# Kernel optimization log

Measured on AMD Instinct MI355X. Metric: run time of the kernel, lower is better.

The kernel has to match this reference:

```python
import jax, jax.numpy as jnp
import numpy as np

B, S, D, H = 16, 577, 1408, 16
HD = D // H  # 88


def setup_inputs() -> dict:
    key = jax.random.key(0)
    k1, k2, k3, k4, k5, k6 = jax.random.split(key, 6)
    hidden_states = jax.random.normal(k1, (B, S, D), dtype=jnp.float32)
    # realistic rotary table: cos/sin pairs stacked in last dim
    theta = jax.random.normal(k2, (S, HD // 2), dtype=jnp.float32)
    freqs_ci = jnp.stack([jnp.cos(theta), jnp.sin(theta)], axis=-1)  # (S, HD/2, 2)
    wqkv = jax.random.normal(k3, (3 * D, D), dtype=jnp.float32) * 0.02
    bqkv = jax.random.normal(k4, (3 * D,), dtype=jnp.float32) * 0.02
    wo = jax.random.normal(k5, (D, D), dtype=jnp.float32) * 0.02
    bo = jax.random.normal(k6, (D,), dtype=jnp.float32) * 0.02
    return {"hidden_states": hidden_states, "freqs_ci": freqs_ci,
            "wqkv": wqkv, "bqkv": bqkv, "wo": wo, "bo": bo}


def reference(hidden_states, freqs_ci, wqkv, bqkv, wo, bo):
    b, s, d = hidden_states.shape
    # fused QKV projection (torch Linear: x @ W.T + b)
    qkv = hidden_states @ wqkv.T + bqkv  # (B, S, 3D)
    q, k, v = jnp.split(qkv, 3, axis=-1)
    q = q.reshape(b, s, H, HD)
    k = k.reshape(b, s, H, HD)
    v = v.reshape(b, s, H, HD)

    cos = freqs_ci[..., 0][None, :, None, :]  # (1, S, 1, HD/2)
    sin = freqs_ci[..., 1][None, :, None, :]

    def rot(x):
        xr = x.reshape(b, s, H, HD // 2, 2)
        xe, xo = xr[..., 0], xr[..., 1]
        re = xe * cos - xo * sin
        ro = xe * sin + xo * cos
        return jnp.stack([re, ro], axis=-1).reshape(b, s, H, HD)

    q = rot(q)
    k = rot(k)

    scale = 1.0 / jnp.sqrt(jnp.float32(HD))  # SDPA default scaling
    scores = jnp.einsum('bqhd,bkhd->bhqk', q, k) * scale
    attn = jax.nn.softmax(scores, axis=-1)
    ctx = jnp.einsum('bhqk,bkhd->bqhd', attn, v).reshape(b, s, d)
    return ctx @ wo.T + bo
```

## Files before the change

kernel.cpp:

```cpp
#include <hip/hip_runtime.h>

typedef __attribute__((ext_vector_type(8))) __bf16 bf16x8;
typedef __attribute__((ext_vector_type(4))) float f32x4;
typedef __attribute__((ext_vector_type(4))) unsigned int uint4v;

#define B_ 16
#define S_ 577
#define D_ 1408
#define H_ 16
#define HD_ 88
#define MROWS (B_*S_)
#define N1 (3*D_)
#define K_ D_
#define KSTEPS 44
#define VT_LD 592
#define QSCALE 0.15379180809f

static __device__ __forceinline__ void async16(void* lds, const void* g) {
  __builtin_amdgcn_global_load_lds((const __attribute__((address_space(1))) void*)g,
                                   (__attribute__((address_space(3))) void*)lds, 16, 0, 0);
}

static __device__ __forceinline__ int xcd_swizzle(int orig, int nwg) {
  int xcd = orig & 7, lid = orig >> 3;
  int q = nwg >> 3, r = nwg & 7;
  return (xcd < r ? xcd * (q + 1) : r * (q + 1) + (xcd - r) * q) + lid;
}

__global__ void cast3_bf16_kernel(const float* __restrict__ s0, __bf16* __restrict__ d0, int n0,
                                  const float* __restrict__ s1, __bf16* __restrict__ d1, int n1,
                                  const float* __restrict__ s2, __bf16* __restrict__ d2, int n2) {
  int i = blockIdx.x * blockDim.x + threadIdx.x;
  const float* s; __bf16* d; int k;
  if (i < n0) { s = s0; d = d0; k = i; }
  else if (i < n0 + n1) { s = s1; d = d1; k = i - n0; }
  else if (i < n0 + n1 + n2) { s = s2; d = d2; k = i - n0 - n1; }
  else return;
  const float4 v = ((const float4*)s)[k];
  __bf16* p = d + (size_t)k * 4;
  p[0] = (__bf16)v.x; p[1] = (__bf16)v.y; p[2] = (__bf16)v.z; p[3] = (__bf16)v.w;
}

__launch_bounds__(256, 2)
__global__ void gemm_qkv_rope(const __bf16* __restrict__ A, const __bf16* __restrict__ Bm,
                              const float* __restrict__ bias, const float* __restrict__ freqs,
                              __bf16* __restrict__ Qb, __bf16* __restrict__ Kb,
                              __bf16* __restrict__ Vb) {
  __shared__ __bf16 As[2][128 * 32];
  __shared__ __bf16 Bs[2][128 * 32];
  const int tid = threadIdx.x;
  const int w = tid >> 6, l = tid & 63;
  const int wgid = xcd_swizzle(blockIdx.x, 33 * 73);
  int mt, nt;
  if (wgid < 2376) { int bnd = wgid / 132, r = wgid % 132; nt = r >> 2; mt = bnd * 4 + (r & 3); }
  else             { nt = wgid - 2376; mt = 72; }
  const int m0 = mt * 128, n0 = nt * 128;
  const int wr = w & 1, wc = w >> 1;
  const int M = MROWS, K = K_;

  f32x4 acc[4][4];
#pragma unroll
  for (int m = 0; m < 4; ++m)
#pragma unroll
    for (int n = 0; n < 4; ++n) acc[m][n] = (f32x4){0.f, 0.f, 0.f, 0.f};

  int arow0 = m0 + w * 32 + (l >> 2);      if (arow0 >= M) arow0 = M - 1;
  int arow1 = m0 + w * 32 + 16 + (l >> 2); if (arow1 >= M) arow1 = M - 1;
  const __bf16* ag0 = A + (size_t)arow0 * K + (l & 3) * 8;
  const __bf16* ag1 = A + (size_t)arow1 * K + (l & 3) * 8;
  const __bf16* bg0 = Bm + (size_t)(n0 + w * 32 + (l >> 2)) * K + (l & 3) * 8;
  const __bf16* bg1 = Bm + (size_t)(n0 + w * 32 + 16 + (l >> 2)) * K + (l & 3) * 8;

  auto stage = [&](int buf, int k0) {
    async16(&As[buf][(w * 32) * 32],      ag0 + k0);
    async16(&As[buf][(w * 32 + 16) * 32], ag1 + k0);
    async16(&Bs[buf][(w * 32) * 32],      bg0 + k0);
    async16(&Bs[buf][(w * 32 + 16) * 32], bg1 + k0);
  };

  stage(0, 0);
  __syncthreads();
  for (int t = 0; t < KSTEPS; ++t) {
    const int cur = t & 1;
    if (t < KSTEPS - 1) stage(cur ^ 1, (t + 1) * 32);
    bf16x8 a[4], b[4];
#pragma unroll
    for (int m = 0; m < 4; ++m)
      a[m] = *(const bf16x8*)&As[cur][(wr * 64 + m * 16 + (l & 15)) * 32 + (l >> 4) * 8];
#pragma unroll
    for (int n = 0; n < 4; ++n)
      b[n] = *(const bf16x8*)&Bs[cur][(wc * 64 + n * 16 + (l & 15)) * 32 + (l >> 4) * 8];
#pragma unroll
    for (int m = 0; m < 4; ++m)
#pragma unroll
      for (int n = 0; n < 4; ++n)
        acc[m][n] = __builtin_amdgcn_mfma_f32_16x16x32_bf16(a[m], b[n], acc[m][n], 0, 0, 0);
    __syncthreads();
  }

  const int sect = n0 / 1408;
  __bf16* dst = (sect == 0) ? Qb : (sect == 1 ? Kb : Vb);
  const float qs = (sect == 0) ? QSCALE : 1.f;
  int hN[4], dN[4], i2N[4];
  float bvN[4], sgnN[4];
#pragma unroll
  for (int n = 0; n < 4; ++n) {
    const int col = n0 + wc * 64 + n * 16 + (l & 15);
    const int cin = col - sect * 1408;
    hN[n] = cin / 88; dN[n] = cin - hN[n] * 88;
    bvN[n] = bias[col];
    i2N[n] = dN[n] & ~1;
    sgnN[n] = (dN[n] & 1) ? 1.f : -1.f;
  }
#pragma unroll
  for (int m = 0; m < 4; ++m) {
    const int rbase = m0 + wr * 64 + m * 16 + (l >> 4) * 4;
#pragma unroll
    for (int j = 0; j < 4; ++j) {
      const int r = rbase + j;
      const int s = r % 577;
      const int b = r / 577;
      const bool ok = r < MROWS;
      const float* frow = freqs + s * 88;
      __bf16* drow = dst + ((size_t)b * 16 * 577 + s) * 88;
#pragma unroll
      for (int n = 0; n < 4; ++n) {
        float val = acc[m][n][j] + bvN[n];
        float outv = val;
        if (sect < 2) {
          const float2 cs = *(const float2*)&frow[i2N[n]];
          const float p = __shfl_xor(val, 1);
          outv = (val * cs.x + sgnN[n] * p * cs.y) * qs;
        }
        if (ok) drow[(size_t)hN[n] * 50776 + dN[n]] = (__bf16)outv;
      }
    }
  }
}

__launch_bounds__(256, 2)
__global__ void gemm_out_bias(const __bf16* __restrict__ A, const __bf16* __restrict__ Bm,
                              const float* __restrict__ bias, float* __restrict__ C) {
  __shared__ __bf16 As[2][128 * 32];
  __shared__ __bf16 Bs[2][128 * 32];
  const int tid = threadIdx.x;
  const int w = tid >> 6, l = tid & 63;
  const int wgid = xcd_swizzle(blockIdx.x, 11 * 73);
  int mt, nt;
  if (wgid < 792) { int bnd = wgid / 44, r = wgid % 44; nt = r >> 2; mt = bnd * 4 + (r & 3); }
  else            { nt = wgid - 792; mt = 72; }
  const int m0 = mt * 128, n0 = nt * 128;
  const int wr = w & 1, wc = w >> 1;
  const int M = MROWS, N = D_, K = K_;

  f32x4 acc[4][4];
#pragma unroll
  for (int m = 0; m < 4; ++m)
#pragma unroll
    for (int n = 0; n < 4; ++n) acc[m][n] = (f32x4){0.f, 0.f, 0.f, 0.f};

  int arow0 = m0 + w * 32 + (l >> 2);      if (arow0 >= M) arow0 = M - 1;
  int arow1 = m0 + w * 32 + 16 + (l >> 2); if (arow1 >= M) arow1 = M - 1;
  const __bf16* ag0 = A + (size_t)arow0 * K + (l & 3) * 8;
  const __bf16* ag1 = A + (size_t)arow1 * K + (l & 3) * 8;
  const __bf16* bg0 = Bm + (size_t)(n0 + w * 32 + (l >> 2)) * K + (l & 3) * 8;
  const __bf16* bg1 = Bm + (size_t)(n0 + w * 32 + 16 + (l >> 2)) * K + (l & 3) * 8;

  auto stage = [&](int buf, int k0) {
    async16(&As[buf][(w * 32) * 32],      ag0 + k0);
    async16(&As[buf][(w * 32 + 16) * 32], ag1 + k0);
    async16(&Bs[buf][(w * 32) * 32],      bg0 + k0);
    async16(&Bs[buf][(w * 32 + 16) * 32], bg1 + k0);
  };

  stage(0, 0);
  __syncthreads();
  for (int t = 0; t < KSTEPS; ++t) {
    const int cur = t & 1;
    if (t < KSTEPS - 1) stage(cur ^ 1, (t + 1) * 32);
    bf16x8 a[4], b[4];
#pragma unroll
    for (int m = 0; m < 4; ++m)
      a[m] = *(const bf16x8*)&As[cur][(wr * 64 + m * 16 + (l & 15)) * 32 + (l >> 4) * 8];
#pragma unroll
    for (int n = 0; n < 4; ++n)
      b[n] = *(const bf16x8*)&Bs[cur][(wc * 64 + n * 16 + (l & 15)) * 32 + (l >> 4) * 8];
#pragma unroll
    for (int m = 0; m < 4; ++m)
#pragma unroll
      for (int n = 0; n < 4; ++n)
        acc[m][n] = __builtin_amdgcn_mfma_f32_16x16x32_bf16(a[m], b[n], acc[m][n], 0, 0, 0);
    __syncthreads();
  }

#pragma unroll
  for (int n = 0; n < 4; ++n) {
    int col = n0 + wc * 64 + n * 16 + (l & 15);
    float bv = bias[col];
#pragma unroll
    for (int m = 0; m < 4; ++m) {
      int rbase = m0 + wr * 64 + m * 16 + (l >> 4) * 4;
#pragma unroll
      for (int j = 0; j < 4; ++j) {
        int r = rbase + j;
        if (r < MROWS) C[(size_t)r * N + col] = acc[m][n][j] + bv;
      }
    }
  }
}

__global__ void transpose_v(const __bf16* __restrict__ V, __bf16* __restrict__ Vt_g) {
  __shared__ __bf16 Ls[64 * 104];
  const int bh = blockIdx.x, t = blockIdx.y, s0 = t * 64;
  const int tid = threadIdx.x;
  const __bf16* vp = V + (size_t)bh * 577 * 88;
  for (int i = tid; i < 64 * 11; i += 256) {
    int r = i / 11, off = i % 11;
    int gs = s0 + r; if (gs > 576) gs = 576;
    *(uint4v*)&Ls[r * 104 + off * 8] = *(const uint4v*)(vp + (size_t)gs * 88 + off * 8);
  }
  __syncthreads();
  for (int i = tid; i < 88 * 8; i += 256) {
    int d = i / 8, so = (i % 8) * 8;
    int sc_ = s0 + so;
    if (sc_ < VT_LD) {
      __bf16 tmp[8];
#pragma unroll
      for (int j = 0; j < 8; ++j) tmp[j] = Ls[(so + j) * 104 + d];
      *(uint4v*)&Vt_g[((size_t)bh * 88 + d) * VT_LD + sc_] = *(uint4v*)tmp;
    }
  }
}

__launch_bounds__(256, 3)
__global__ void attn_kernel(const __bf16* __restrict__ Q, const __bf16* __restrict__ K,
                            const __bf16* __restrict__ Vt_gp, __bf16* __restrict__ ctx) {
  __shared__ __bf16 lds[26368];
  const int tid = threadIdx.x;
  const int w = tid >> 6, l = tid & 63;
  const int bh = blockIdx.x;
  const int q0 = blockIdx.y * 128;
  const __bf16* qp = Q + (size_t)bh * 577 * 88;
  const __bf16* kp = K + (size_t)bh * 577 * 88;
  const __bf16* vtp = Vt_gp + (size_t)bh * 88 * VT_LD;
  __bf16* Qs = lds;
  __bf16* Ks = lds + 12288;
  __bf16* Vt = lds + 17920;
  __bf16* Pw = lds + w * 2304;

  for (int i = tid; i < 128 * 11; i += 256) {
    int r = i / 11, off = i % 11;
    int gr = q0 + r; if (gr > 576) gr = 576;
    *(uint4v*)&Qs[r * 96 + off * 8] = *(const uint4v*)(qp + (size_t)gr * 88 + off * 8);
  }
  if (tid < 128) { uint4v z = 0; *(uint4v*)&Qs[tid * 96 + 88] = z; }
  __syncthreads();

  bf16x8 qf[2][3];
#pragma unroll
  for (int mg = 0; mg < 2; ++mg)
#pragma unroll
    for (int kk = 0; kk < 3; ++kk)
      qf[mg][kk] = *(const bf16x8*)&Qs[(w * 32 + mg * 16 + (l & 15)) * 96 + kk * 32 + (l >> 4) * 8];

  int preA[7], preB[7];
#pragma unroll
  for (int kch = 0; kch < 7; ++kch) {
    int c = w + 4 * kch;
    int a = 0, b2 = 0;
    if (c < 11) a = c * 512 + l * 8;
    else if (c < 27) { int e = (c - 11) * 512 + l * 8; a = (e / 88) * VT_LD; b2 = e % 88; }
    preA[kch] = a; preB[kch] = b2;
  }

  f32x4 oacc[2][6];
#pragma unroll
  for (int mg = 0; mg < 2; ++mg)
#pragma unroll
    for (int dn = 0; dn < 6; ++dn) oacc[mg][dn] = (f32x4){0.f, 0.f, 0.f, 0.f};
  f32x4 mrun[2], lrun[2];
  mrun[0] = -1e30f; mrun[1] = -1e30f;
  lrun[0] = 0.f; lrun[1] = 0.f;

  for (int t = 0; t < 10; ++t) {
    const int s0 = t * 64;
    if (t) __syncthreads();
#pragma unroll
    for (int kch = 0; kch < 7; ++kch) {
      int c = w + 4 * kch;
      if (c < 11) {
        async16(Ks + c * 512, kp + (size_t)s0 * 88 + preA[kch]);
      } else if (c < 27) {
        int g = s0 + preB[kch]; if (g > 584) g = 584;
        async16(Vt + (c - 11) * 512, vtp + preA[kch] + g);
      }
    }
    __syncthreads();

    f32x4 sc[2][4];
#pragma unroll
    for (int mg = 0; mg < 2; ++mg)
#pragma unroll
      for (int n = 0; n < 4; ++n) sc[mg][n] = (f32x4){0.f, 0.f, 0.f, 0.f};
#pragma unroll
    for (int n = 0; n < 4; ++n) {
#pragma unroll
      for (int kk = 0; kk < 3; ++kk) {
        bf16x8 kf = *(const bf16x8*)&Ks[(n * 16 + (l & 15)) * 88 + kk * 32 + (l >> 4) * 8];
        sc[0][n] = __builtin_amdgcn_mfma_f32_16x16x32_bf16(qf[0][kk], kf, sc[0][n], 0, 0, 0);
        sc[1][n] = __builtin_amdgcn_mfma_f32_16x16x32_bf16(qf[1][kk], kf, sc[1][n], 0, 0, 0);
      }
    }

    f32x4 tmax[2];
    tmax[0] = -1e30f; tmax[1] = -1e30f;
#pragma unroll
    for (int n = 0; n < 4; ++n) {
      const int kc = s0 + n * 16 + (l & 15);
      const bool valid = kc < 577;
#pragma unroll
      for (int mg = 0; mg < 2; ++mg)
#pragma unroll
        for (int j = 0; j < 4; ++j) {
          float v = valid ? sc[mg][n][j] : -1e30f;
          sc[mg][n][j] = v;
          tmax[mg][j] = fmaxf(tmax[mg][j], v);
        }
    }
#pragma unroll
    for (int o = 1; o < 16; o <<= 1)
#pragma unroll
      for (int mg = 0; mg < 2; ++mg)
#pragma unroll
        for (int j = 0; j < 4; ++j)
          tmax[mg][j] = fmaxf(tmax[mg][j], __shfl_xor(tmax[mg][j], o));

    bool need = false;
#pragma unroll
    for (int mg = 0; mg < 2; ++mg)
#pragma unroll
      for (int j = 0; j < 4; ++j)
        need = need || (tmax[mg][j] > mrun[mg][j] + 8.f);
    if (__any(need)) {
#pragma unroll
      for (int mg = 0; mg < 2; ++mg)
#pragma unroll
        for (int j = 0; j < 4; ++j) {
          float mo = mrun[mg][j];
          float mn = fmaxf(mo, tmax[mg][j]);
          float sf = exp2f(mo - mn);
          mrun[mg][j] = mn;
          lrun[mg][j] *= sf;
#pragma unroll
          for (int dn = 0; dn < 6; ++dn) oacc[mg][dn][j] *= sf;
        }
    }
#pragma unroll
    for (int mg = 0; mg < 2; ++mg)
#pragma unroll
      for (int n = 0; n < 4; ++n)
#pragma unroll
        for (int j = 0; j < 4; ++j) {
          float p = exp2f(sc[mg][n][j] - mrun[mg][j]);
          lrun[mg][j] += p;
          Pw[(mg * 16 + (l >> 4) * 4 + j) * 72 + n * 16 + (l & 15)] = (__bf16)p;
        }

#pragma unroll
    for (int ks = 0; ks < 2; ++ks) {
      bf16x8 pa0 = *(const bf16x8*)&Pw[((l & 15)) * 72 + ks * 32 + (l >> 4) * 8];
      bf16x8 pa1 = *(const bf16x8*)&Pw[(16 + (l & 15)) * 72 + ks * 32 + (l >> 4) * 8];
#pragma unroll
      for (int dn = 0; dn < 6; ++dn) {
        bf16x8 vb = *(const bf16x8*)&Vt[(dn * 16 + (l & 15)) * 88 + ks * 32 + (l >> 4) * 8];
        oacc[0][dn] = __builtin_amdgcn_mfma_f32_16x16x32_bf16(pa0, vb, oacc[0][dn], 0, 0, 0);
        oacc[1][dn] = __builtin_amdgcn_mfma_f32_16x16x32_bf16(pa1, vb, oacc[1][dn], 0, 0, 0);
      }
    }
  }

#pragma unroll
  for (int o = 1; o < 16; o <<= 1)
#pragma unroll
    for (int mg = 0; mg < 2; ++mg)
#pragma unroll
      for (int j = 0; j < 4; ++j)
        lrun[mg][j] += __shfl_xor(lrun[mg][j], o);

  const int b = bh >> 4, h = bh & 15;
#pragma unroll
  for (int mg = 0; mg < 2; ++mg) {
    float inv[4];
#pragma unroll
    for (int j = 0; j < 4; ++j) inv[j] = 1.f / lrun[mg][j];
    const int sqb = q0 + w * 32 + mg * 16 + (l >> 4) * 4;
#pragma unroll
    for (int dn = 0; dn < 6; ++dn) {
      const int d = dn * 16 + (l & 15);
      if (d >= 88) continue;
#pragma unroll
      for (int j = 0; j < 4; ++j) {
        const int sq = sqb + j;
        if (sq < 577)
          ctx[((size_t)(b * 577 + sq)) * 1408 + h * 88 + d] = (__bf16)(oacc[mg][dn][j] * inv[j]);
      }
    }
  }
}

extern "C" void kernel_launch(void* const* d_in, const int* in_sizes, int n_in,
                              void* d_out, int out_size, void* d_ws, size_t ws_size,
                              hipStream_t stream) {
  const float* hs    = (const float*)d_in[0];
  const float* freqs = (const float*)d_in[1];
  const float* wqkv  = (const float*)d_in[2];
  const float* bqkv  = (const float*)d_in[3];
  const float* wo    = (const float*)d_in[4];
  const float* bo    = (const float*)d_in[5];
  float* out = (float*)d_out;

  char* ws = (char*)d_ws;
  size_t off = 0;
  auto alloc = [&](size_t bytes) {
    void* p = ws + off;
    off += (bytes + 255) & ~(size_t)255;
    return p;
  };
  __bf16* x_bf    = (__bf16*)alloc((size_t)MROWS * K_ * 2);
  __bf16* ctx_bf  = x_bf;
  __bf16* wqkv_bf = (__bf16*)alloc((size_t)N1 * K_ * 2);
  __bf16* wo_bf   = (__bf16*)alloc((size_t)D_ * K_ * 2);
  __bf16* q_bf    = (__bf16*)alloc((size_t)MROWS * D_ * 2);
  __bf16* k_bf    = (__bf16*)alloc((size_t)MROWS * D_ * 2);
  __bf16* v_bf    = (__bf16*)alloc((size_t)MROWS * D_ * 2);
  __bf16* vt_g    = (__bf16*)d_out;

  const int n0 = MROWS * K_ / 4, n1 = N1 * K_ / 4, n2 = D_ * K_ / 4;
  cast3_bf16_kernel<<<(n0 + n1 + n2 + 255) / 256, 256, 0, stream>>>(
      hs, x_bf, n0, wqkv, wqkv_bf, n1, wo, wo_bf, n2);

  gemm_qkv_rope<<<33 * 73, 256, 0, stream>>>(x_bf, wqkv_bf, bqkv, freqs, q_bf, k_bf, v_bf);

  transpose_v<<<dim3(256, 10), 256, 0, stream>>>(v_bf, vt_g);

  attn_kernel<<<dim3(256, 5), 256, 0, stream>>>(q_bf, k_bf, vt_g, ctx_bf);

  gemm_out_bias<<<11 * 73, 256, 0, stream>>>(ctx_bf, wo_bf, bo, out);
}
```

Baseline: 387.3 us.

## Prefetch next K/V tile into registers while computing attention

Replaces the per-tile direct global-to-LDS async loads, which were issued and then waited on right away, with a software pipeline. Each thread loads the next K and Vt tile into registers during the current tile's MFMA and softmax work, then writes them to LDS after the barrier. The aim is to hide global memory latency behind compute. In exchange it adds about 24 VGPRs of prefetch state under a 3-blocks-per-CU launch bound, and it drops the old column clamp on Vt reads.

```diff
diff --git a/kernel.cpp b/kernel.cpp
--- a/kernel.cpp
+++ b/kernel.cpp
@@ -248,6 +248,21 @@
   __bf16* Vt = lds + 17920;
   __bf16* Pw = lds + w * 2304;
 
+  int ki[3], vdo[3], vco[3];
+#pragma unroll
+  for (int k3 = 0; k3 < 3; ++k3) {
+    int i = tid + k3 * 256; if (i > 703) i = 703;
+    ki[k3] = i * 8;
+    vdo[k3] = i >> 3; vco[k3] = (i & 7) * 8;
+  }
+
+  uint4v kr[3], vr[3];
+#pragma unroll
+  for (int k3 = 0; k3 < 3; ++k3) {
+    kr[k3] = *(const uint4v*)(kp + ki[k3]);
+    vr[k3] = *(const uint4v*)(vtp + (size_t)vdo[k3] * VT_LD + vco[k3]);
+  }
+
   for (int i = tid; i < 128 * 11; i += 256) {
     int r = i / 11, off = i % 11;
     int gr = q0 + r; if (gr > 576) gr = 576;
@@ -263,16 +278,6 @@
     for (int kk = 0; kk < 3; ++kk)
       qf[mg][kk] = *(const bf16x8*)&Qs[(w * 32 + mg * 16 + (l & 15)) * 96 + kk * 32 + (l >> 4) * 8];
 
-  int preA[7], preB[7];
-#pragma unroll
-  for (int kch = 0; kch < 7; ++kch) {
-    int c = w + 4 * kch;
-    int a = 0, b2 = 0;
-    if (c < 11) a = c * 512 + l * 8;
-    else if (c < 27) { int e = (c - 11) * 512 + l * 8; a = (e / 88) * VT_LD; b2 = e % 88; }
-    preA[kch] = a; preB[kch] = b2;
-  }
-
   f32x4 oacc[2][6];
 #pragma unroll
   for (int mg = 0; mg < 2; ++mg)
@@ -286,16 +291,19 @@
     const int s0 = t * 64;
     if (t) __syncthreads();
 #pragma unroll
-    for (int kch = 0; kch < 7; ++kch) {
-      int c = w + 4 * kch;
-      if (c < 11) {
-        async16(Ks + c * 512, kp + (size_t)s0 * 88 + preA[kch]);
-      } else if (c < 27) {
-        int g = s0 + preB[kch]; if (g > 584) g = 584;
-        async16(Vt + (c - 11) * 512, vtp + preA[kch] + g);
-      }
+    for (int k3 = 0; k3 < 3; ++k3) {
+      *(uint4v*)(Ks + ki[k3]) = kr[k3];
+      *(uint4v*)(Vt + vdo[k3] * 88 + vco[k3]) = vr[k3];
     }
     __syncthreads();
+    if (t < 9) {
+      const int s0n = s0 + 64;
+#pragma unroll
+      for (int k3 = 0; k3 < 3; ++k3) {
+        kr[k3] = *(const uint4v*)(kp + (size_t)s0n * 88 + ki[k3]);
+        vr[k3] = *(const uint4v*)(vtp + (size_t)vdo[k3] * VT_LD + s0n + vco[k3]);
+      }
+    }
 
     f32x4 sc[2][4];
 #pragma unroll
```

After: 421.5 us. 1.09x slower.

## Triple-buffer GEMM LDS staging with explicit vmcnt waits and raw barriers

Applied to the files above, without the earlier changes.

Both bf16 GEMM kernels (QKV+RoPE and output projection) move from a double-buffered to a triple-buffered LDS pipeline that keeps two K-tiles of async global-to-LDS loads in flight. The full __syncthreads drains are replaced by explicit s_waitcnt vmcnt(8) / lgkmcnt(0) plus sched barriers and raw s_barrier, so the wait only covers the oldest tile. This is meant to hide global load latency better, at the cost of 50% more LDS (48KB per block), which may pressure occupancy at 2 blocks/CU. The tail iterations redundantly reload the last tile.

```diff
diff --git a/kernel.cpp b/kernel.cpp
--- a/kernel.cpp
+++ b/kernel.cpp
@@ -26,6 +26,12 @@
   int q = nwg >> 3, r = nwg & 7;
   return (xcd < r ? xcd * (q + 1) : r * (q + 1) + (xcd - r) * q) + lid;
 }
+
+#define SB0() __builtin_amdgcn_sched_barrier(0)
+#define LGKM0() do { asm volatile("s_waitcnt lgkmcnt(0)" ::: "memory"); SB0(); } while (0)
+#define VMW8()  do { asm volatile("s_waitcnt vmcnt(8)" ::: "memory"); SB0(); } while (0)
+#define VMDRAIN() asm volatile("s_waitcnt vmcnt(0)" ::: "memory")
+#define BARR() do { SB0(); __builtin_amdgcn_s_barrier(); SB0(); } while (0)
 
 __global__ void cast3_bf16_kernel(const float* __restrict__ s0, __bf16* __restrict__ d0, int n0,
                                   const float* __restrict__ s1, __bf16* __restrict__ d1, int n1,
@@ -46,8 +52,8 @@
                               const float* __restrict__ bias, const float* __restrict__ freqs,
                               __bf16* __restrict__ Qb, __bf16* __restrict__ Kb,
                               __bf16* __restrict__ Vb) {
-  __shared__ __bf16 As[2][128 * 32];
-  __shared__ __bf16 Bs[2][128 * 32];
+  __shared__ __bf16 As[3][128 * 32];
+  __shared__ __bf16 Bs[3][128 * 32];
   const int tid = threadIdx.x;
   const int w = tid >> 6, l = tid & 63;
   const int wgid = xcd_swizzle(blockIdx.x, 33 * 73);
@@ -79,10 +85,13 @@
   };
 
   stage(0, 0);
-  __syncthreads();
+  stage(1, 32);
   for (int t = 0; t < KSTEPS; ++t) {
-    const int cur = t & 1;
-    if (t < KSTEPS - 1) stage(cur ^ 1, (t + 1) * 32);
+    int kn = t + 2; if (kn > KSTEPS - 1) kn = KSTEPS - 1;
+    stage((t + 2) % 3, kn * 32);
+    VMW8();
+    BARR();
+    const int cur = t % 3;
     bf16x8 a[4], b[4];
 #pragma unroll
     for (int m = 0; m < 4; ++m)
@@ -95,8 +104,10 @@
 #pragma unroll
       for (int n = 0; n < 4; ++n)
         acc[m][n] = __builtin_amdgcn_mfma_f32_16x16x32_bf16(a[m], b[n], acc[m][n], 0, 0, 0);
-    __syncthreads();
-  }
+    LGKM0();
+    BARR();
+  }
+  VMDRAIN();
 
   const int sect = n0 / 1408;
   __bf16* dst = (sect == 0) ? Qb : (sect == 1 ? Kb : Vb);
@@ -141,8 +152,8 @@
 __launch_bounds__(256, 2)
 __global__ void gemm_out_bias(const __bf16* __restrict__ A, const __bf16* __restrict__ Bm,
                               const float* __restrict__ bias, float* __restrict__ C) {
-  __shared__ __bf16 As[2][128 * 32];
-  __shared__ __bf16 Bs[2][128 * 32];
+  __shared__ __bf16 As[3][128 * 32];
+  __shared__ __bf16 Bs[3][128 * 32];
   const int tid = threadIdx.x;
   const int w = tid >> 6, l = tid & 63;
   const int wgid = xcd_swizzle(blockIdx.x, 11 * 73);
@@ -174,10 +185,13 @@
   };
 
   stage(0, 0);
-  __syncthreads();
+  stage(1, 32);
   for (int t = 0; t < KSTEPS; ++t) {
-    const int cur = t & 1;
-    if (t < KSTEPS - 1) stage(cur ^ 1, (t + 1) * 32);
+    int kn = t + 2; if (kn > KSTEPS - 1) kn = KSTEPS - 1;
+    stage((t + 2) % 3, kn * 32);
+    VMW8();
+    BARR();
+    const int cur = t % 3;
     bf16x8 a[4], b[4];
 #pragma unroll
     for (int m = 0; m < 4; ++m)
@@ -190,8 +204,10 @@
 #pragma unroll
       for (int n = 0; n < 4; ++n)
         acc[m][n] = __builtin_amdgcn_mfma_f32_16x16x32_bf16(a[m], b[n], acc[m][n], 0, 0, 0);
-    __syncthreads();
-  }
+    LGKM0();
+    BARR();
+  }
+  VMDRAIN();
 
 #pragma unroll
   for (int n = 0; n < 4; ++n) {
```

Measured after the change: 419.8 us. 1.08x slower.
